# Performance work log

Hardware: AMD Instinct MI355X
Metric: run time of the kernel (lower is better)

## Reference

```python
import jax, jax.numpy as jnp
import numpy as np

B, T, D = 16, 8192, 512
NHEAD, NKV = 8, 2
HD = D // NHEAD            # 64
KV_DIM = NKV * HD          # 128
N_REP = NHEAD // NKV       # 4
SCALE = 1.0 / np.sqrt(HD)


def setup_inputs() -> dict:
    key = jax.random.key(0)
    ks = jax.random.split(key, 8)
    w = 0.02
    return {
        "query": jax.random.normal(ks[0], (B, D), dtype=jnp.float32),
        "enc": jax.random.normal(ks[1], (B, T, D), dtype=jnp.float32),
        "Wq": jax.random.normal(ks[2], (D, D), dtype=jnp.float32) * w,
        "Wk": jax.random.normal(ks[3], (D, KV_DIM), dtype=jnp.float32) * w,
        "Wv": jax.random.normal(ks[4], (D, KV_DIM), dtype=jnp.float32) * w,
        "W1": jax.random.normal(ks[5], (2 * D, 4 * D), dtype=jnp.float32) * w,
        "W2": jax.random.normal(ks[6], (4 * D, D), dtype=jnp.float32) * w,
    }


def reference(query, enc, Wq, Wk, Wv, W1, W2):
    # Q projection: single decoder step -> [B, H, HD]
    q = (query @ Wq).reshape(B, NHEAD, HD)
    # K/V projections (GQA): [B, T, NKV, HD] -> [B, NKV, T, HD]
    k = (enc @ Wk).reshape(B, T, NKV, HD).transpose(0, 2, 1, 3)
    v = (enc @ Wv).reshape(B, T, NKV, HD).transpose(0, 2, 1, 3)
    # repeat KV heads to match query heads: [B, H, T, HD]
    k = jnp.repeat(k, N_REP, axis=1)
    v = jnp.repeat(v, N_REP, axis=1)
    # scaled dot-product attention, Tq == 1
    scores = jnp.einsum("bhd,bhtd->bht", q, k) * SCALE        # [B, H, T]
    attn = jax.nn.softmax(scores, axis=-1)
    context = jnp.einsum("bht,bhtd->bhd", attn, v).reshape(B, D)
    # combine context with query through SwiGLU-style MLP (Linear-SiLU-Linear)
    h = jnp.concatenate([context, query], axis=-1)            # [B, 2D]
    out = jax.nn.silu(h @ W1) @ W2                            # [B, D]
    return out
```

## Files before the change

### kernel.cpp

```cpp
#include <hip/hip_runtime.h>
#include <hip/hip_bf16.h>
#include <cstdint>
#include <cstddef>

#define BB 16
#define TT 8192
#define DD 512
#define NHEAD 8
#define NKV 2
#define HD 64
#define KVD 128
#define SCALE 0.125f
#define QSCALE 0.18033688011112042f

#define RB 64
#define NCHUNK (TT / RB)
#define BK 32
#define NSTEP (DD / BK)

typedef __attribute__((ext_vector_type(8))) short bf16x8;
typedef __attribute__((ext_vector_type(4))) float f32x4;

#define WS_Q      0
#define WS_WBT    8192
#define WS_OPART  73728
#define WS_ML     1122304
#define WS_H      1155072
#define WS_APART  1171456
#define WS_M2     1728512

__device__ __forceinline__ ushort f2bf(float f) {
    uint u = __builtin_bit_cast(uint, f);
    u += 0x7fffu + ((u >> 16) & 1u);
    return (ushort)(u >> 16);
}
__device__ __forceinline__ uint cvtpk(float a, float b) {
    uint r;
    asm("v_cvt_pk_bf16_f32 %0, %1, %2" : "=v"(r) : "v"(a), "v"(b));
    return r;
}
__device__ __forceinline__ float bf1(ushort s) {
    return __builtin_bit_cast(float, (uint)s << 16);
}
__device__ __forceinline__ float bflo(uint u) {
    return __builtin_bit_cast(float, u << 16);
}
__device__ __forceinline__ float bfhi(uint u) {
    return __builtin_bit_cast(float, u & 0xffff0000u);
}

__global__ __launch_bounds__(256) void k_prep(const float* __restrict__ Wk,
                                              const float* __restrict__ Wv,
                                              const float* __restrict__ query,
                                              const float* __restrict__ Wq,
                                              ushort* __restrict__ wbt4,
                                              float* __restrict__ wsq) {
    const int t = threadIdx.x;
    if (blockIdx.x < 64) {
        const int G0 = blockIdx.x * 2048 + t * 8;
        const int s = G0 >> 13, r = G0 & 8191;
        const int fid = r >> 9, lane = (r >> 3) & 63;
        const int col = (fid >> 2) * 64 + (fid & 3) * 16 + (lane & 15);
        const int kbase = s * 32 + (lane >> 4) * 8;
        const float* W = (col < KVD) ? (Wk + col) : (Wv + (col - KVD));
#pragma unroll
        for (int e = 0; e < 8; ++e)
            wbt4[G0 + e] = f2bf(W[(size_t)(kbase + e) * KVD]);
    } else {
        __shared__ float qrow[DD];
        const int x = blockIdx.x - 64;
        const int b = x >> 1, half = x & 1;
        qrow[t] = query[b * DD + t];
        qrow[t + 256] = query[b * DD + t + 256];
        __syncthreads();
        const int col = half * 256 + t;
        float a0 = 0.f;
#pragma unroll 8
        for (int d = 0; d < DD; ++d) a0 = fmaf(qrow[d], Wq[(size_t)d * DD + col], a0);
        wsq[b * DD + col] = a0;
    }
}

__global__ __launch_bounds__(256) void k_attn(const float* __restrict__ enc,
                                              const ushort* __restrict__ wbt4,
                                              const float* __restrict__ wsq,
                                              float* __restrict__ o_part,
                                              float* __restrict__ ml) {
    __shared__ __align__(16) char smem[33024];
    __shared__ float sc[NHEAD * RB];
    __shared__ float qs[DD];

    const int tid = threadIdx.x;
    const int chunk = blockIdx.x, b = blockIdx.y;
    const int lane = tid & 63, w = tid >> 6;

    qs[tid] = wsq[b * DD + tid] * QSCALE;
    qs[tid + 256] = wsq[b * DD + tid + 256] * QSCALE;

    char* const A0 = smem;
    char* const A1 = smem + 4096;
    ushort* const kvl = (ushort*)smem;

    const float* encb = enc + ((size_t)b * TT + (size_t)chunk * RB) * DD;
    const ushort* wfr = wbt4 + ((size_t)w * 256 + lane) * 8;

    const int srow = (tid >> 6) * 16 + (tid & 15);
    const int skb = ((tid >> 4) & 3) * 8;

    f32x4 acc[4][4];
#pragma unroll
    for (int i = 0; i < 4; ++i)
#pragma unroll
        for (int j = 0; j < 4; ++j) acc[i][j] = (f32x4){0.f, 0.f, 0.f, 0.f};

    float4 eA0, eA1, eB0, eB1;
    bf16x8 bfA[4], bfB[4], af[4];

#define LOAD_E(E0, E1, ss)                                                           \
    {                                                                                \
        const float* p_ = encb + (size_t)srow * DD + (ss) * BK + skb;                \
        E0 = *(const float4*)p_;                                                     \
        E1 = *(const float4*)(p_ + 4);                                               \
    }
#define WRITE_A(Abuf, E0, E1)                                                        \
    {                                                                                \
        uint4 u_;                                                                    \
        u_.x = cvtpk(E0.x, E0.y);                                                    \
        u_.y = cvtpk(E0.z, E0.w);                                                    \
        u_.z = cvtpk(E1.x, E1.y);                                                    \
        u_.w = cvtpk(E1.z, E1.w);                                                    \
        *(uint4*)((Abuf) + tid * 16) = u_;                                           \
    }
#define LOAD_B(BF, ss)                                                               \
    {                                                                                \
        _Pragma("unroll") for (int nt = 0; nt < 4; ++nt)                             \
            BF[nt] = *(const bf16x8*)(wfr + (size_t)(ss) * 8192 + nt * 512);         \
    }
#define SYNC()                                                                       \
    {                                                                                \
        __builtin_amdgcn_sched_barrier(0);                                           \
        asm volatile("s_waitcnt lgkmcnt(0)" ::: "memory");                           \
        __builtin_amdgcn_s_barrier();                                                \
    }
#define MFMA_STEP(Ac, BF)                                                            \
    {                                                                                \
        _Pragma("unroll") for (int rt = 0; rt < 4; ++rt)                             \
            af[rt] = *(const bf16x8*)((Ac) + (rt * 64 + lane) * 16);                 \
        _Pragma("unroll") for (int rt = 0; rt < 4; ++rt)                             \
            _Pragma("unroll") for (int nt = 0; nt < 4; ++nt)                         \
                acc[rt][nt] = __builtin_amdgcn_mfma_f32_16x16x32_bf16(               \
                    af[rt], BF[nt], acc[rt][nt], 0, 0, 0);                           \
    }

    LOAD_E(eA0, eA1, 0);
    LOAD_B(bfA, 0);
    LOAD_E(eB0, eB1, 1);
    WRITE_A(A0, eA0, eA1);
    LOAD_E(eA0, eA1, 2);
    SYNC();

#pragma unroll
    for (int s = 0; s < NSTEP; ++s) {
        char* const Ac = (s & 1) ? A1 : A0;
        char* const An = (s & 1) ? A0 : A1;
        if ((s & 1) == 0) {
            if (s + 1 < NSTEP) WRITE_A(An, eB0, eB1);
            if (s + 3 < NSTEP) LOAD_E(eB0, eB1, s + 3);
            if (s + 1 < NSTEP) LOAD_B(bfB, s + 1);
            MFMA_STEP(Ac, bfA);
        } else {
            if (s + 1 < NSTEP) WRITE_A(An, eA0, eA1);
            if (s + 3 < NSTEP) LOAD_E(eA0, eA1, s + 3);
            if (s + 1 < NSTEP) LOAD_B(bfA, s + 1);
            MFMA_STEP(Ac, bfB);
        }
        SYNC();
    }

    const int h0 = w * 2;
    const int kvh = h0 >> 2;

    __syncthreads();
#pragma unroll
    for (int rt = 0; rt < 4; ++rt)
#pragma unroll
        for (int nt = 0; nt < 4; ++nt) {
            const int col = w * 64 + nt * 16 + (lane & 15);
#pragma unroll
            for (int j = 0; j < 4; ++j) {
                const int row = rt * 16 + (lane >> 4) * 4 + j;
                kvl[row * 258 + col] = f2bf(acc[rt][nt][j]);
            }
        }
    __syncthreads();

    {
        const float* qh0 = qs + h0 * HD;
        const float* qh1 = qs + (h0 + 1) * HD;
        const uint* kr = (const uint*)(kvl + lane * 258 + kvh * HD);
        float s0 = 0.f, s1 = 0.f;
#pragma unroll
        for (int d2 = 0; d2 < 32; ++d2) {
            const uint u = kr[d2];
            const float klo = bflo(u), khi = bfhi(u);
            s0 = fmaf(klo, qh0[2 * d2], s0);
            s0 = fmaf(khi, qh0[2 * d2 + 1], s0);
            s1 = fmaf(klo, qh1[2 * d2], s1);
            s1 = fmaf(khi, qh1[2 * d2 + 1], s1);
        }
        sc[h0 * RB + lane] = s0;
        sc[(h0 + 1) * RB + lane] = s1;
    }
    __syncthreads();

    {
        float mx0 = -1e30f, mx1 = -1e30f;
#pragma unroll 8
        for (int r = 0; r < RB; ++r) {
            mx0 = fmaxf(mx0, sc[h0 * RB + r]);
            mx1 = fmaxf(mx1, sc[(h0 + 1) * RB + r]);
        }
        float l0 = 0.f, l1 = 0.f, o0 = 0.f, o1 = 0.f;
        const ushort* vcol = kvl + KVD + kvh * HD + lane;
#pragma unroll 4
        for (int r = 0; r < RB; ++r) {
            const float vv = bf1(vcol[r * 258]);
            const float p0 = exp2f(sc[h0 * RB + r] - mx0);
            const float p1 = exp2f(sc[(h0 + 1) * RB + r] - mx1);
            l0 += p0; o0 = fmaf(p0, vv, o0);
            l1 += p1; o1 = fmaf(p1, vv, o1);
        }
        const size_t base0 = ((size_t)b * NCHUNK + chunk) * NHEAD + h0;
        o_part[base0 * HD + lane] = o0;
        o_part[(base0 + 1) * HD + lane] = o1;
        if (lane == 0) {
            ml[base0 * 2] = mx0; ml[base0 * 2 + 1] = l0;
            ml[(base0 + 1) * 2] = mx1; ml[(base0 + 1) * 2 + 1] = l1;
        }
    }
#undef LOAD_E
#undef WRITE_A
#undef LOAD_B
#undef SYNC
#undef MFMA_STEP
}

__global__ __launch_bounds__(512) void k_reduce(const float* __restrict__ o_part,
                                                const float* __restrict__ ml,
                                                const float* __restrict__ query,
                                                float* __restrict__ hvec) {
    __shared__ float sEl[NHEAD][NCHUNK];
    const int b = blockIdx.x, t = threadIdx.x;
    const int h = t >> 6, lane = t & 63;

    const size_t ma_i = (((size_t)b * NCHUNK + lane) * NHEAD + h) * 2;
    const size_t mb_i = (((size_t)b * NCHUNK + lane + 64) * NHEAD + h) * 2;
    const float ma = ml[ma_i], la = ml[ma_i + 1];
    const float mb = ml[mb_i], lb = ml[mb_i + 1];
    float M = fmaxf(ma, mb);
#pragma unroll
    for (int off = 32; off >= 1; off >>= 1) M = fmaxf(M, __shfl_xor(M, off));
    const float ea = exp2f(ma - M), eb = exp2f(mb - M);
    float L = la * ea + lb * eb;
#pragma unroll
    for (int off = 32; off >= 1; off >>= 1) L += __shfl_xor(L, off);
    sEl[h][lane] = ea;
    sEl[h][lane + 64] = eb;
    __syncthreads();

    float O = 0.f;
#pragma unroll 4
    for (int i = 0; i < NCHUNK; ++i) {
        const size_t base = ((size_t)b * NCHUNK + i) * NHEAD + h;
        O = fmaf(o_part[base * HD + lane], sEl[h][i], O);
    }
    hvec[b * 1024 + h * HD + lane] = O / L;
    hvec[b * 1024 + 512 + t] = query[b * DD + t];
}

__global__ __launch_bounds__(256) void k_mlp1(const float* __restrict__ hvec,
                                              const float* __restrict__ W1,
                                              float* __restrict__ apart) {
    const int jb = blockIdx.x, ib = blockIdx.y;
    const int j = jb * 256 + threadIdx.x;
    float acc[BB];
#pragma unroll
    for (int b = 0; b < BB; ++b) acc[b] = 0.f;
    for (int i0 = ib * 64; i0 < ib * 64 + 64; i0 += 4) {
        const float w0 = W1[(size_t)(i0 + 0) * 2048 + j];
        const float w1 = W1[(size_t)(i0 + 1) * 2048 + j];
        const float w2 = W1[(size_t)(i0 + 2) * 2048 + j];
        const float w3 = W1[(size_t)(i0 + 3) * 2048 + j];
#pragma unroll
        for (int b = 0; b < BB; ++b) {
            const float* hb = hvec + b * 1024 + i0;
            acc[b] = fmaf(hb[0], w0, acc[b]);
            acc[b] = fmaf(hb[1], w1, acc[b]);
            acc[b] = fmaf(hb[2], w2, acc[b]);
            acc[b] = fmaf(hb[3], w3, acc[b]);
        }
    }
#pragma unroll
    for (int b = 0; b < BB; ++b)
        apart[((size_t)ib * BB + b) * 2048 + j] = acc[b];
}

__global__ __launch_bounds__(256) void k_mlp2(const float* __restrict__ apart,
                                              const float* __restrict__ W2,
                                              float* __restrict__ m2part) {
    __shared__ float actl[256];
    const int jb = blockIdx.x, b = blockIdx.y, ib = blockIdx.z;
    const int t = threadIdx.x;
    {
        const int jglob = ib * 256 + t;
        float s = 0.f;
#pragma unroll
        for (int p = 0; p < 16; ++p) s += apart[((size_t)p * BB + b) * 2048 + jglob];
        actl[t] = s / (1.f + __expf(-s));
    }
    __syncthreads();
    const int d = jb * 256 + t;
    float acc = 0.f;
    for (int j0 = 0; j0 < 256; j0 += 4) {
        const int jg = ib * 256 + j0;
        acc = fmaf(actl[j0 + 0], W2[(size_t)(jg + 0) * 512 + d], acc);
        acc = fmaf(actl[j0 + 1], W2[(size_t)(jg + 1) * 512 + d], acc);
        acc = fmaf(actl[j0 + 2], W2[(size_t)(jg + 2) * 512 + d], acc);
        acc = fmaf(actl[j0 + 3], W2[(size_t)(jg + 3) * 512 + d], acc);
    }
    m2part[((size_t)ib * BB + b) * 512 + d] = acc;
}

__global__ __launch_bounds__(512) void k_out(const float* __restrict__ m2part,
                                             float* __restrict__ out) {
    const int b = blockIdx.x, t = threadIdx.x;
    float s = 0.f;
#pragma unroll
    for (int ib = 0; ib < 8; ++ib) s += m2part[((size_t)ib * BB + b) * 512 + t];
    out[b * DD + t] = s;
}

extern "C" void kernel_launch(void* const* d_in, const int* in_sizes, int n_in,
                              void* d_out, int out_size, void* d_ws, size_t ws_size,
                              hipStream_t stream) {
    const float* query = (const float*)d_in[0];
    const float* enc   = (const float*)d_in[1];
    const float* Wq    = (const float*)d_in[2];
    const float* Wk    = (const float*)d_in[3];
    const float* Wv    = (const float*)d_in[4];
    const float* W1    = (const float*)d_in[5];
    const float* W2    = (const float*)d_in[6];
    float* ws  = (float*)d_ws;
    float* out = (float*)d_out;
    ushort* wbt4 = (ushort*)(ws + WS_WBT);

    k_prep<<<dim3(96), dim3(256), 0, stream>>>(Wk, Wv, query, Wq, wbt4, ws + WS_Q);
    k_attn<<<dim3(NCHUNK, BB), dim3(256), 0, stream>>>(enc, wbt4, ws + WS_Q,
                                                       ws + WS_OPART, ws + WS_ML);
    k_reduce<<<dim3(BB), dim3(512), 0, stream>>>(ws + WS_OPART, ws + WS_ML, query, ws + WS_H);
    k_mlp1<<<dim3(8, 16), dim3(256), 0, stream>>>(ws + WS_H, W1, ws + WS_APART);
    k_mlp2<<<dim3(2, BB, 8), dim3(256), 0, stream>>>(ws + WS_APART, W2, ws + WS_M2);
    k_out<<<dim3(BB), dim3(512), 0, stream>>>(ws + WS_M2, out);
}
```

Measured before the change: 146.7 us.

## Repartition KV projection GEMM so each wave owns 16 rows, dropping LDS staging

```diff
diff --git a/kernel.cpp b/kernel.cpp
--- a/kernel.cpp
+++ b/kernel.cpp
@@ -38,6 +38,14 @@
     uint r;
     asm("v_cvt_pk_bf16_f32 %0, %1, %2" : "=v"(r) : "v"(a), "v"(b));
     return r;
+}
+__device__ __forceinline__ bf16x8 pack8(float4 a, float4 b) {
+    uint4 u;
+    u.x = cvtpk(a.x, a.y);
+    u.y = cvtpk(a.z, a.w);
+    u.z = cvtpk(b.x, b.y);
+    u.w = cvtpk(b.z, b.w);
+    return __builtin_bit_cast(bf16x8, u);
 }
 __device__ __forceinline__ float bf1(ushort s) {
     return __builtin_bit_cast(float, (uint)s << 16);
@@ -86,7 +94,7 @@
                                               const float* __restrict__ wsq,
                                               float* __restrict__ o_part,
                                               float* __restrict__ ml) {
-    __shared__ __align__(16) char smem[33024];
+    __shared__ ushort kvl[RB * 258];
     __shared__ float sc[NHEAD * RB];
     __shared__ float qs[DD];
 
@@ -97,101 +105,54 @@
     qs[tid] = wsq[b * DD + tid] * QSCALE;
     qs[tid + 256] = wsq[b * DD + tid + 256] * QSCALE;
 
-    char* const A0 = smem;
-    char* const A1 = smem + 4096;
-    ushort* const kvl = (ushort*)smem;
-
-    const float* encb = enc + ((size_t)b * TT + (size_t)chunk * RB) * DD;
-    const ushort* wfr = wbt4 + ((size_t)w * 256 + lane) * 8;
-
-    const int srow = (tid >> 6) * 16 + (tid & 15);
-    const int skb = ((tid >> 4) & 3) * 8;
-
-    f32x4 acc[4][4];
-#pragma unroll
-    for (int i = 0; i < 4; ++i)
-#pragma unroll
-        for (int j = 0; j < 4; ++j) acc[i][j] = (f32x4){0.f, 0.f, 0.f, 0.f};
-
-    float4 eA0, eA1, eB0, eB1;
-    bf16x8 bfA[4], bfB[4], af[4];
-
-#define LOAD_E(E0, E1, ss)                                                           \
-    {                                                                                \
-        const float* p_ = encb + (size_t)srow * DD + (ss) * BK + skb;                \
-        E0 = *(const float4*)p_;                                                     \
-        E1 = *(const float4*)(p_ + 4);                                               \
-    }
-#define WRITE_A(Abuf, E0, E1)                                                        \
-    {                                                                                \
-        uint4 u_;                                                                    \
-        u_.x = cvtpk(E0.x, E0.y);                                                    \
-        u_.y = cvtpk(E0.z, E0.w);                                                    \
-        u_.z = cvtpk(E1.x, E1.y);                                                    \
-        u_.w = cvtpk(E1.z, E1.w);                                                    \
-        *(uint4*)((Abuf) + tid * 16) = u_;                                           \
-    }
-#define LOAD_B(BF, ss)                                                               \
-    {                                                                                \
-        _Pragma("unroll") for (int nt = 0; nt < 4; ++nt)                             \
-            BF[nt] = *(const bf16x8*)(wfr + (size_t)(ss) * 8192 + nt * 512);         \
-    }
-#define SYNC()                                                                       \
-    {                                                                                \
-        __builtin_amdgcn_sched_barrier(0);                                           \
-        asm volatile("s_waitcnt lgkmcnt(0)" ::: "memory");                           \
-        __builtin_amdgcn_s_barrier();                                                \
-    }
-#define MFMA_STEP(Ac, BF)                                                            \
-    {                                                                                \
-        _Pragma("unroll") for (int rt = 0; rt < 4; ++rt)                             \
-            af[rt] = *(const bf16x8*)((Ac) + (rt * 64 + lane) * 16);                 \
-        _Pragma("unroll") for (int rt = 0; rt < 4; ++rt)                             \
-            _Pragma("unroll") for (int nt = 0; nt < 4; ++nt)                         \
-                acc[rt][nt] = __builtin_amdgcn_mfma_f32_16x16x32_bf16(               \
-                    af[rt], BF[nt], acc[rt][nt], 0, 0, 0);                           \
-    }
-
-    LOAD_E(eA0, eA1, 0);
-    LOAD_B(bfA, 0);
-    LOAD_E(eB0, eB1, 1);
-    WRITE_A(A0, eA0, eA1);
-    LOAD_E(eA0, eA1, 2);
-    SYNC();
+    const float* arow = enc + ((size_t)b * TT + (size_t)chunk * RB + w * 16 +
+                               (lane & 15)) * DD + (lane >> 4) * 8;
+    const ushort* wb = wbt4 + (size_t)lane * 8;
+
+    f32x4 acc[16];
+#pragma unroll
+    for (int i = 0; i < 16; ++i) acc[i] = (f32x4){0.f, 0.f, 0.f, 0.f};
+
+    float4 pA0, pA1, pB0, pB1;
+    pA0 = *(const float4*)(arow);
+    pA1 = *(const float4*)(arow + 4);
 
 #pragma unroll
     for (int s = 0; s < NSTEP; ++s) {
-        char* const Ac = (s & 1) ? A1 : A0;
-        char* const An = (s & 1) ? A0 : A1;
+        bf16x8 af;
         if ((s & 1) == 0) {
-            if (s + 1 < NSTEP) WRITE_A(An, eB0, eB1);
-            if (s + 3 < NSTEP) LOAD_E(eB0, eB1, s + 3);
-            if (s + 1 < NSTEP) LOAD_B(bfB, s + 1);
-            MFMA_STEP(Ac, bfA);
+            if (s + 1 < NSTEP) {
+                pB0 = *(const float4*)(arow + (s + 1) * BK);
+                pB1 = *(const float4*)(arow + (s + 1) * BK + 4);
+            }
+            af = pack8(pA0, pA1);
         } else {
-            if (s + 1 < NSTEP) WRITE_A(An, eA0, eA1);
-            if (s + 3 < NSTEP) LOAD_E(eA0, eA1, s + 3);
-            if (s + 1 < NSTEP) LOAD_B(bfA, s + 1);
-            MFMA_STEP(Ac, bfB);
-        }
-        SYNC();
+            if (s + 1 < NSTEP) {
+                pA0 = *(const float4*)(arow + (s + 1) * BK);
+                pA1 = *(const float4*)(arow + (s + 1) * BK + 4);
+            }
+            af = pack8(pB0, pB1);
+        }
+        const ushort* wbs = wb + (size_t)s * 8192;
+#pragma unroll
+        for (int nt = 0; nt < 16; ++nt) {
+            const bf16x8 bfr = *(const bf16x8*)(wbs + nt * 512);
+            acc[nt] = __builtin_amdgcn_mfma_f32_16x16x32_bf16(af, bfr, acc[nt], 0, 0, 0);
+        }
     }
 
     const int h0 = w * 2;
     const int kvh = h0 >> 2;
 
-    __syncthreads();
-#pragma unroll
-    for (int rt = 0; rt < 4; ++rt)
-#pragma unroll
-        for (int nt = 0; nt < 4; ++nt) {
-            const int col = w * 64 + nt * 16 + (lane & 15);
-#pragma unroll
-            for (int j = 0; j < 4; ++j) {
-                const int row = rt * 16 + (lane >> 4) * 4 + j;
-                kvl[row * 258 + col] = f2bf(acc[rt][nt][j]);
-            }
-        }
+#pragma unroll
+    for (int nt = 0; nt < 16; ++nt) {
+        const int col = (nt >> 2) * 64 + (nt & 3) * 16 + (lane & 15);
+#pragma unroll
+        for (int j = 0; j < 4; ++j) {
+            const int row = w * 16 + (lane >> 4) * 4 + j;
+            kvl[row * 258 + col] = f2bf(acc[nt][j]);
+        }
+    }
     __syncthreads();
 
     {
@@ -238,11 +199,6 @@
             ml[(base0 + 1) * 2] = mx1; ml[(base0 + 1) * 2 + 1] = l1;
         }
     }
-#undef LOAD_E
-#undef WRITE_A
-#undef LOAD_B
-#undef SYNC
-#undef MFMA_STEP
 }
 
 __global__ __launch_bounds__(512) void k_reduce(const float* __restrict__ o_part,
```

Measured after the change: 294.4 us. +100.7%, slower.
